# Kernel optimization log

Measured on AMD Instinct MI355X. Metric: run time of the kernel, lower is better.

## Reference

```python
import jax, jax.numpy as jnp
import numpy as np

B, L, U = 64, 512, 7          # batch, seq_len, enc_in
H = 128                        # hidden_dim
LAYERS = 2                     # num LSTM layers
PRED = 96                      # pred_len
EPS = 1e-5


def setup_inputs() -> dict:
    key = jax.random.key(0)
    ks = jax.random.split(key, 9)
    s = 0.05  # small param scale for numerical sanity
    return {
        "x": jax.random.normal(ks[0], (B, L, U), dtype=jnp.float32),
        "emb_W": jax.random.normal(ks[1], (H, 1), dtype=jnp.float32) * s,
        "emb_b": jax.random.normal(ks[2], (H,), dtype=jnp.float32) * s,
        "Wih": jax.random.normal(ks[3], (LAYERS, 4 * H, H), dtype=jnp.float32) * s,
        "Whh": jax.random.normal(ks[4], (LAYERS, 4 * H, H), dtype=jnp.float32) * s,
        "bih": jax.random.normal(ks[5], (LAYERS, 4 * H), dtype=jnp.float32) * s,
        "bhh": jax.random.normal(ks[6], (LAYERS, 4 * H), dtype=jnp.float32) * s,
        "fc_W": jax.random.normal(ks[7], (PRED, H), dtype=jnp.float32) * s,
        "fc_b": jax.random.normal(ks[8], (PRED,), dtype=jnp.float32) * s,
    }


def _lstm_layer(x, Wih, Whh, bih, bhh):
    """PyTorch-semantics single LSTM layer. x: [N, L, H_in] -> [N, L, H]."""
    N = x.shape[0]
    Hh = Whh.shape[1]
    # precompute input projections for all timesteps: [N, L, 4H]
    xp = jnp.einsum('nli,gi->nlg', x, Wih) + bih + bhh
    xp = jnp.swapaxes(xp, 0, 1)  # [L, N, 4H] for scan over time

    def step(carry, xt):
        h, c = carry
        gates = xt + h @ Whh.T           # [N, 4H]
        i, f, g, o = jnp.split(gates, 4, axis=-1)  # torch gate order i,f,g,o
        i = jax.nn.sigmoid(i)
        f = jax.nn.sigmoid(f)
        g = jnp.tanh(g)
        o = jax.nn.sigmoid(o)
        c = f * c + i * g
        h = o * jnp.tanh(c)
        return (h, c), h

    h0 = jnp.zeros((N, Hh), x.dtype)
    (_, _), hs = jax.lax.scan(step, (h0, h0), xp)
    return jnp.swapaxes(hs, 0, 1)  # [N, L, H]


def reference(x, emb_W, emb_b, Wih, Whh, bih, bhh, fc_W, fc_b):
    Bn, Ln, Un = x.shape
    # per-channel instance norm over time (stats detached in original)
    means = jax.lax.stop_gradient(jnp.mean(x, axis=1, keepdims=True))          # [B,1,U]
    stdev = jax.lax.stop_gradient(jnp.sqrt(jnp.var(x, axis=1, keepdims=True) + EPS))
    xn = (x - means) / stdev
    # NOTE: original does a raw row-major reshape (no channel permute); replicate exactly.
    xs = xn.reshape(Bn * Un, Ln, 1)                                            # [B*U, L, 1]
    h = xs @ emb_W.T + emb_b                                                   # [B*U, L, H]
    for l in range(Wih.shape[0]):
        h = _lstm_layer(h, Wih[l], Whh[l], bih[l], bhh[l])
    out = h[:, -1, :] @ fc_W.T + fc_b                                          # [B*U, PRED]
    out = out.reshape(Bn, -1, Un)                                              # [B, PRED, U]
    return out * stdev + means
```

## Files before the change

### kernel.cpp

```cpp
#include <hip/hip_runtime.h>
#include <stdint.h>

typedef short bf16x8 __attribute__((ext_vector_type(8)));
typedef float f32x4  __attribute__((ext_vector_type(4)));

#define HH 128
#define NN 448
#define PREDN 96

#define OFF_MEAN 0
#define OFF_STD  448
#define OFF_A    896
#define OFF_B0   1408
#define OFF_B1   1920
#define OFF_H1   2432
#define OFF_XSB  59776
#define OFF_WPK  174464

#define L2E  1.442695041f
#define L2E2 2.885390082f

#define ROWB 592
#define BUFB 9472

__device__ __forceinline__ float bflo(uint32_t w){ union{uint32_t u; float f;} v; v.u = w<<16; return v.f; }
__device__ __forceinline__ float bfhi(uint32_t w){ union{uint32_t u; float f;} v; v.u = w & 0xffff0000u; return v.f; }

static __device__ __forceinline__ uint32_t packbf2(float a, float b){
    union { float f; uint32_t u; } ua, ub; ua.f = a; ub.f = b;
    uint32_t x = ua.u, y = ub.u;
    uint32_t lo = (x + 0x7fffu + ((x>>16)&1u)) >> 16;
    uint32_t hi = (y + 0x7fffu + ((y>>16)&1u)) >> 16;
    return (lo & 0xffffu) | (hi<<16);
}
static __device__ __forceinline__ uint16_t bfr(float f){
    union { float f; uint32_t u; } v; v.f = f;
    return (uint16_t)((v.u + 0x7fffu + ((v.u>>16)&1u)) >> 16);
}

#if __has_builtin(__builtin_amdgcn_exp2f)
#define EXP2(x) __builtin_amdgcn_exp2f(x)
#else
#define EXP2(x) __expf(0.69314718056f*(x))
#endif
#if __has_builtin(__builtin_amdgcn_rcpf)
#define RCPF(x) __builtin_amdgcn_rcpf(x)
#else
#define RCPF(x) (1.0f/(x))
#endif

__device__ __forceinline__ float sig2(float x){ return RCPF(1.f + EXP2(-x)); }
__device__ __forceinline__ float tanh2(float xs){ return fmaf(-2.f, RCPF(EXP2(xs) + 1.f), 1.f); }

__global__ void stats_k(const float* __restrict__ x, float* __restrict__ ws){
    int bu = blockIdx.x;
    int b = bu / 7, u = bu % 7;
    int i = threadIdx.x;
    const float* p = x + b*3584 + u;
    float s = 0.f, q = 0.f;
    #pragma unroll
    for (int m=0;m<8;m++){ float v = p[(i + 64*m)*7]; s += v; q += v*v; }
    for (int o=32;o>0;o>>=1){ s += __shfl_down(s,o); q += __shfl_down(q,o); }
    if (i==0){
        float mean = s * (1.f/512.f);
        float var  = q * (1.f/512.f) - mean*mean;
        ws[OFF_MEAN + bu] = mean;
        ws[OFF_STD  + bu] = sqrtf(var + 1e-5f);
    }
}

__global__ void norm_k(const float* __restrict__ x, float* __restrict__ ws){
    int i = blockIdx.x*256 + threadIdx.x;
    int b = i / 3584, u = i % 7;
    float m = ws[OFF_MEAN + b*7 + u];
    float sd = ws[OFF_STD + b*7 + u];
    float v = (x[i] - m) / sd;
    int np = i >> 9, tp = i & 511;
    uint16_t* xb = (uint16_t*)(ws + OFF_XSB);
    xb[(np>>4)*8192 + tp*16 + (np&15)] = (uint16_t)(packbf2(v, 0.f) & 0xffffu);
}

__global__ void prep_k(const float* __restrict__ Wih, const float* __restrict__ embW,
                       const float* __restrict__ embb, const float* __restrict__ bih,
                       const float* __restrict__ bhh, float* __restrict__ ws){
    int g = threadIdx.x;
    const float* wr = Wih + g*HH;
    float a = 0.f, bb = 0.f;
    #pragma unroll 4
    for (int k=0;k<HH;k++){ a += wr[k]*embW[k]; bb += wr[k]*embb[k]; }
    ws[OFF_A  + g] = a;
    ws[OFF_B0 + g] = bb + bih[g] + bhh[g];
    ws[OFF_B1 + g] = bih[512 + g] + bhh[512 + g];
}

__global__ void prep2_k(const float* __restrict__ Whh, const float* __restrict__ Wih,
                        float* __restrict__ ws){
    int idx = blockIdx.x*256 + threadIdx.x;
    int lane = idx & 63;
    int sg = idx >> 6;
    int wvmt = sg / 13, slot = sg % 13;
    int gp  = wvmt*16 + (lane&15);
    int type = gp & 3, unit = gp >> 2;
    int row = type*128 + unit;
    float S = (type==2) ? L2E2 : L2E;
    uint4 r;
    if (slot == 4){
        r.x = r.y = r.z = r.w = 0u;
        if ((lane>>4) == 0) r.x = packbf2(ws[OFF_A+row]*S, ws[OFF_B0+row]*S);
    } else {
        const float* src; int kk;
        if (slot < 4)      { src = Whh + row*128;         kk = slot;   }
        else if (slot < 9) { src = Wih + 65536 + row*128; kk = slot-5; }
        else               { src = Whh + 65536 + row*128; kk = slot-9; }
        int k0 = kk*32 + (lane>>4)*8;
        r.x = packbf2(src[k0]*S,   src[k0+1]*S);
        r.y = packbf2(src[k0+2]*S, src[k0+3]*S);
        r.z = packbf2(src[k0+4]*S, src[k0+5]*S);
        r.w = packbf2(src[k0+6]*S, src[k0+7]*S);
    }
    ((uint4*)(ws + OFF_WPK))[sg*64 + lane] = r;
}

union FragU { bf16x8 v; uint4 q; };

__device__ __forceinline__ f32x4 mm(bf16x8 a, bf16x8 b, f32x4 c){
    return __builtin_amdgcn_mfma_f32_16x16x32_bf16(a, b, c, 0, 0, 0);
}
#define LD(p) (*(const bf16x8*)(p))

__global__ __launch_bounds__(512, 2) void lstm_core(float* __restrict__ ws)
{
    __shared__ uint16_t xsT[8192];
    __shared__ __align__(16) uint16_t hbuf[2*BUFB/2];

    const int tid = threadIdx.x;
    const int wv = tid>>6, l = tid&63;
    const int r   = l & 15;
    const int q16 = (l>>4)*16;
    const int bx = blockIdx.x, n0 = bx*16;
    char* hb = (char*)hbuf;

    const uint16_t* xb = (const uint16_t*)(ws + OFF_XSB) + bx*8192;
    for (int i=tid;i<8192;i+=512) xsT[i] = xb[i];
    for (int i=tid;i<BUFB;i+=512) hbuf[i] = 0;
    __syncthreads();
    if (tid < 32){
        int bsel = tid>>4, rr = tid&15;
        *(uint16_t*)(hb + bsel*BUFB + rr*ROWB + 514) = 0x3F80;
    }
    if (tid < 16){
        *(uint16_t*)(hb + tid*ROWB + 512) = xsT[tid];
    }

    bf16x8 wL0[4][5], wI1[4][4], wH1[4][4];
    uint32_t b1pk[4][2];
    const uint4* wpk = (const uint4*)(ws + OFF_WPK);
    #pragma unroll
    for (int mt=0;mt<4;++mt){
        int base = ((wv*4+mt)*13)*64 + l;
        #pragma unroll
        for (int kk=0;kk<5;kk++){ FragU u; u.q = wpk[base + kk*64];     wL0[mt][kk]=u.v; }
        #pragma unroll
        for (int kk=0;kk<4;kk++){ FragU u; u.q = wpk[base + (5+kk)*64]; wI1[mt][kk]=u.v; }
        #pragma unroll
        for (int kk=0;kk<4;kk++){ FragU u; u.q = wpk[base + (9+kk)*64]; wH1[mt][kk]=u.v; }
        int uu = (wv*4+mt)*4 + (l>>4);
        b1pk[mt][0] = packbf2(ws[OFF_B1+uu]*L2E,      ws[OFF_B1+128+uu]*L2E);
        b1pk[mt][1] = packbf2(ws[OFF_B1+256+uu]*L2E2, ws[OFF_B1+384+uu]*L2E);
    }

    float c0[4]={0,0,0,0}, c1[4]={0,0,0,0};
    const int rbase = r*ROWB + q16;
    const int wbase = r*ROWB + wv*32 + 2*(l>>4);

    __syncthreads();

    for (int t=0;t<512;++t){
        const int co = (t&1)*BUFB;
        const int no = BUFB - co;
        const char* pc = hb + co + rbase;
        const char* pn = hb + no + rbase;
        char* pw = hb + no + wbase;

        {
            bf16x8 f0 = LD(pc+0), f1 = LD(pc+64), f2 = LD(pc+128), f3 = LD(pc+192), fa = LD(pc+512);
            f32x4 a0={0,0,0,0}, a1={0,0,0,0}, a2={0,0,0,0}, a3={0,0,0,0};
            a0=mm(wL0[0][0],f0,a0); a1=mm(wL0[1][0],f0,a1); a2=mm(wL0[2][0],f0,a2); a3=mm(wL0[3][0],f0,a3);
            a0=mm(wL0[0][1],f1,a0); a1=mm(wL0[1][1],f1,a1); a2=mm(wL0[2][1],f1,a2); a3=mm(wL0[3][1],f1,a3);
            a0=mm(wL0[0][2],f2,a0); a1=mm(wL0[1][2],f2,a1); a2=mm(wL0[2][2],f2,a2); a3=mm(wL0[3][2],f2,a3);
            a0=mm(wL0[0][3],f3,a0); a1=mm(wL0[1][3],f3,a1); a2=mm(wL0[2][3],f3,a2); a3=mm(wL0[3][3],f3,a3);
            a0=mm(wL0[0][4],fa,a0); a1=mm(wL0[1][4],fa,a1); a2=mm(wL0[2][4],fa,a2); a3=mm(wL0[3][4],fa,a3);
            #pragma unroll
            for (int mt=0;mt<4;++mt){
                f32x4 a = (mt==0)?a0:(mt==1)?a1:(mt==2)?a2:a3;
                float i_ = sig2(a[0]);
                float f_ = sig2(a[1]);
                float g_ = tanh2(a[2]);
                float o_ = sig2(a[3]);
                float cn = fmaf(f_, c0[mt], i_*g_);
                c0[mt] = cn;
                float h = o_ * tanh2(cn*L2E2);
                *(uint16_t*)(pw + 8*mt) = bfr(h);
            }
        }
        __syncthreads();

        {
            bf16x8 g0 = LD(pn+0),   g1 = LD(pn+64),  g2 = LD(pn+128), g3 = LD(pn+192);
            bf16x8 v0 = LD(pc+256), v1 = LD(pc+320), v2 = LD(pc+384), v3 = LD(pc+448);
            f32x4 a0={0,0,0,0}, a1={0,0,0,0}, a2={0,0,0,0}, a3={0,0,0,0};
            a0=mm(wI1[0][0],g0,a0); a1=mm(wI1[1][0],g0,a1); a2=mm(wI1[2][0],g0,a2); a3=mm(wI1[3][0],g0,a3);
            a0=mm(wI1[0][1],g1,a0); a1=mm(wI1[1][1],g1,a1); a2=mm(wI1[2][1],g1,a2); a3=mm(wI1[3][1],g1,a3);
            a0=mm(wI1[0][2],g2,a0); a1=mm(wI1[1][2],g2,a1); a2=mm(wI1[2][2],g2,a2); a3=mm(wI1[3][2],g2,a3);
            a0=mm(wI1[0][3],g3,a0); a1=mm(wI1[1][3],g3,a1); a2=mm(wI1[2][3],g3,a2); a3=mm(wI1[3][3],g3,a3);
            a0=mm(wH1[0][0],v0,a0); a1=mm(wH1[1][0],v0,a1); a2=mm(wH1[2][0],v0,a2); a3=mm(wH1[3][0],v0,a3);
            a0=mm(wH1[0][1],v1,a0); a1=mm(wH1[1][1],v1,a1); a2=mm(wH1[2][1],v1,a2); a3=mm(wH1[3][1],v1,a3);
            a0=mm(wH1[0][2],v2,a0); a1=mm(wH1[1][2],v2,a1); a2=mm(wH1[2][2],v2,a2); a3=mm(wH1[3][2],v2,a3);
            a0=mm(wH1[0][3],v3,a0); a1=mm(wH1[1][3],v3,a1); a2=mm(wH1[2][3],v3,a2); a3=mm(wH1[3][3],v3,a3);
            #pragma unroll
            for (int mt=0;mt<4;++mt){
                f32x4 a = (mt==0)?a0:(mt==1)?a1:(mt==2)?a2:a3;
                float i_ = sig2(a[0] + bflo(b1pk[mt][0]));
                float f_ = sig2(a[1] + bfhi(b1pk[mt][0]));
                float g_ = tanh2(a[2] + bflo(b1pk[mt][1]));
                float o_ = sig2(a[3] + bfhi(b1pk[mt][1]));
                float cn = fmaf(f_, c1[mt], i_*g_);
                c1[mt] = cn;
                float h = o_ * tanh2(cn*L2E2);
                *(uint16_t*)(pw + 256 + 8*mt) = bfr(h);
                if (t==511) ws[OFF_H1 + (n0+r)*128 + (wv*16 + mt*4 + (l>>4))] = h;
            }
        }
        if (wv==0 && l<16){
            *(uint16_t*)(hb + no + l*ROWB + 512) = xsT[((t+1)&511)*16 + l];
        }
        __syncthreads();
    }
}

__global__ void out_k(const float* __restrict__ fcW, const float* __restrict__ fcb,
                      const float* __restrict__ ws, float* __restrict__ out){
    __shared__ float hl[128];
    int n = blockIdx.x, tid = threadIdx.x;
    hl[tid] = ws[OFF_H1 + n*128 + tid];
    __syncthreads();
    if (tid < PREDN){
        float acc = fcb[tid];
        const float* wr = fcW + tid*128;
        #pragma unroll 4
        for (int k=0;k<128;k++) acc += wr[k]*hl[k];
        int idx = n*PREDN + tid;
        int b = idx / 672, u = idx % 7;
        out[idx] = acc * ws[OFF_STD + b*7 + u] + ws[OFF_MEAN + b*7 + u];
    }
}

extern "C" void kernel_launch(void* const* d_in, const int* in_sizes, int n_in,
                              void* d_out, int out_size, void* d_ws, size_t ws_size,
                              hipStream_t stream)
{
    const float* x    = (const float*)d_in[0];
    const float* embW = (const float*)d_in[1];
    const float* embb = (const float*)d_in[2];
    const float* Wih  = (const float*)d_in[3];
    const float* Whh  = (const float*)d_in[4];
    const float* bih  = (const float*)d_in[5];
    const float* bhh  = (const float*)d_in[6];
    const float* fcW  = (const float*)d_in[7];
    const float* fcb  = (const float*)d_in[8];
    float* ws  = (float*)d_ws;
    float* out = (float*)d_out;

    stats_k<<<448, 64, 0, stream>>>(x, ws);
    norm_k<<<896, 256, 0, stream>>>(x, ws);
    prep_k<<<1, 512, 0, stream>>>(Wih, embW, embb, bih, bhh, ws);
    prep2_k<<<104, 256, 0, stream>>>(Whh, Wih, ws);
    lstm_core<<<28, 512, 0, stream>>>(ws);
    out_k<<<NN, 128, 0, stream>>>(fcW, fcb, ws, out);
}
```

Measured before the change: 1.003 ms.

## Skew LSTM layers by one timestep to remove per-step barrier

Layer 1 now processes timestep t-1 while layer 0 processes timestep t, so both read the same current h buffer and one __syncthreads per step is dropped. A separate epilogue finishes the last layer-1 step and writes the final hidden state. It also adds s_setprio around the MFMA blocks and a sched_barrier to steer instruction scheduling. The risk is correctness at the skew boundaries: the t==0 layer-1 update is skipped and the final step is handled outside the loop.

```diff
diff --git a/kernel.cpp b/kernel.cpp
--- a/kernel.cpp
+++ b/kernel.cpp
@@ -131,7 +131,7 @@
 __global__ __launch_bounds__(512, 2) void lstm_core(float* __restrict__ ws)
 {
     __shared__ uint16_t xsT[8192];
-    __shared__ __align__(16) uint16_t hbuf[2*BUFB/2];
+    __shared__ __align__(16) uint16_t hbuf[BUFB];
 
     const int tid = threadIdx.x;
     const int wv = tid>>6, l = tid&63;
@@ -179,47 +179,50 @@
         const int co = (t&1)*BUFB;
         const int no = BUFB - co;
         const char* pc = hb + co + rbase;
-        const char* pn = hb + no + rbase;
         char* pw = hb + no + wbase;
 
-        {
-            bf16x8 f0 = LD(pc+0), f1 = LD(pc+64), f2 = LD(pc+128), f3 = LD(pc+192), fa = LD(pc+512);
-            f32x4 a0={0,0,0,0}, a1={0,0,0,0}, a2={0,0,0,0}, a3={0,0,0,0};
-            a0=mm(wL0[0][0],f0,a0); a1=mm(wL0[1][0],f0,a1); a2=mm(wL0[2][0],f0,a2); a3=mm(wL0[3][0],f0,a3);
-            a0=mm(wL0[0][1],f1,a0); a1=mm(wL0[1][1],f1,a1); a2=mm(wL0[2][1],f1,a2); a3=mm(wL0[3][1],f1,a3);
-            a0=mm(wL0[0][2],f2,a0); a1=mm(wL0[1][2],f2,a1); a2=mm(wL0[2][2],f2,a2); a3=mm(wL0[3][2],f2,a3);
-            a0=mm(wL0[0][3],f3,a0); a1=mm(wL0[1][3],f3,a1); a2=mm(wL0[2][3],f3,a2); a3=mm(wL0[3][3],f3,a3);
-            a0=mm(wL0[0][4],fa,a0); a1=mm(wL0[1][4],fa,a1); a2=mm(wL0[2][4],fa,a2); a3=mm(wL0[3][4],fa,a3);
+        bf16x8 f0 = LD(pc+0), f1 = LD(pc+64), f2 = LD(pc+128), f3 = LD(pc+192);
+        f32x4 b0={0,0,0,0}, b1={0,0,0,0}, b2={0,0,0,0}, b3={0,0,0,0};
+        __builtin_amdgcn_s_setprio(1);
+        b0=mm(wI1[0][0],f0,b0); b1=mm(wI1[1][0],f0,b1); b2=mm(wI1[2][0],f0,b2); b3=mm(wI1[3][0],f0,b3);
+        b0=mm(wI1[0][1],f1,b0); b1=mm(wI1[1][1],f1,b1); b2=mm(wI1[2][1],f1,b2); b3=mm(wI1[3][1],f1,b3);
+        b0=mm(wI1[0][2],f2,b0); b1=mm(wI1[1][2],f2,b1); b2=mm(wI1[2][2],f2,b2); b3=mm(wI1[3][2],f2,b3);
+        b0=mm(wI1[0][3],f3,b0); b1=mm(wI1[1][3],f3,b1); b2=mm(wI1[2][3],f3,b2); b3=mm(wI1[3][3],f3,b3);
+        bf16x8 fa = LD(pc+512);
+        f32x4 a0={0,0,0,0}, a1={0,0,0,0}, a2={0,0,0,0}, a3={0,0,0,0};
+        a0=mm(wL0[0][0],f0,a0); a1=mm(wL0[1][0],f0,a1); a2=mm(wL0[2][0],f0,a2); a3=mm(wL0[3][0],f0,a3);
+        a0=mm(wL0[0][1],f1,a0); a1=mm(wL0[1][1],f1,a1); a2=mm(wL0[2][1],f1,a2); a3=mm(wL0[3][1],f1,a3);
+        a0=mm(wL0[0][2],f2,a0); a1=mm(wL0[1][2],f2,a1); a2=mm(wL0[2][2],f2,a2); a3=mm(wL0[3][2],f2,a3);
+        a0=mm(wL0[0][3],f3,a0); a1=mm(wL0[1][3],f3,a1); a2=mm(wL0[2][3],f3,a2); a3=mm(wL0[3][3],f3,a3);
+        a0=mm(wL0[0][4],fa,a0); a1=mm(wL0[1][4],fa,a1); a2=mm(wL0[2][4],fa,a2); a3=mm(wL0[3][4],fa,a3);
+        __builtin_amdgcn_s_setprio(0);
+
+        #pragma unroll
+        for (int mt=0;mt<4;++mt){
+            f32x4 a = (mt==0)?a0:(mt==1)?a1:(mt==2)?a2:a3;
+            float i_ = sig2(a[0]);
+            float f_ = sig2(a[1]);
+            float g_ = tanh2(a[2]);
+            float o_ = sig2(a[3]);
+            float cn = fmaf(f_, c0[mt], i_*g_);
+            c0[mt] = cn;
+            float h = o_ * tanh2(cn*L2E2);
+            *(uint16_t*)(pw + 8*mt) = bfr(h);
+        }
+
+        __builtin_amdgcn_sched_barrier(0);
+        bf16x8 v0 = LD(pc+256), v1 = LD(pc+320), v2 = LD(pc+384), v3 = LD(pc+448);
+        __builtin_amdgcn_s_setprio(1);
+        b0=mm(wH1[0][0],v0,b0); b1=mm(wH1[1][0],v0,b1); b2=mm(wH1[2][0],v0,b2); b3=mm(wH1[3][0],v0,b3);
+        b0=mm(wH1[0][1],v1,b0); b1=mm(wH1[1][1],v1,b1); b2=mm(wH1[2][1],v1,b2); b3=mm(wH1[3][1],v1,b3);
+        b0=mm(wH1[0][2],v2,b0); b1=mm(wH1[1][2],v2,b1); b2=mm(wH1[2][2],v2,b2); b3=mm(wH1[3][2],v2,b3);
+        b0=mm(wH1[0][3],v3,b0); b1=mm(wH1[1][3],v3,b1); b2=mm(wH1[2][3],v3,b2); b3=mm(wH1[3][3],v3,b3);
+        __builtin_amdgcn_s_setprio(0);
+
+        if (t){
             #pragma unroll
             for (int mt=0;mt<4;++mt){
-                f32x4 a = (mt==0)?a0:(mt==1)?a1:(mt==2)?a2:a3;
-                float i_ = sig2(a[0]);
-                float f_ = sig2(a[1]);
-                float g_ = tanh2(a[2]);
-                float o_ = sig2(a[3]);
-                float cn = fmaf(f_, c0[mt], i_*g_);
-                c0[mt] = cn;
-                float h = o_ * tanh2(cn*L2E2);
-                *(uint16_t*)(pw + 8*mt) = bfr(h);
-            }
-        }
-        __syncthreads();
-
-        {
-            bf16x8 g0 = LD(pn+0),   g1 = LD(pn+64),  g2 = LD(pn+128), g3 = LD(pn+192);
-            bf16x8 v0 = LD(pc+256), v1 = LD(pc+320), v2 = LD(pc+384), v3 = LD(pc+448);
-            f32x4 a0={0,0,0,0}, a1={0,0,0,0}, a2={0,0,0,0}, a3={0,0,0,0};
-            a0=mm(wI1[0][0],g0,a0); a1=mm(wI1[1][0],g0,a1); a2=mm(wI1[2][0],g0,a2); a3=mm(wI1[3][0],g0,a3);
-            a0=mm(wI1[0][1],g1,a0); a1=mm(wI1[1][1],g1,a1); a2=mm(wI1[2][1],g1,a2); a3=mm(wI1[3][1],g1,a3);
-            a0=mm(wI1[0][2],g2,a0); a1=mm(wI1[1][2],g2,a1); a2=mm(wI1[2][2],g2,a2); a3=mm(wI1[3][2],g2,a3);
-            a0=mm(wI1[0][3],g3,a0); a1=mm(wI1[1][3],g3,a1); a2=mm(wI1[2][3],g3,a2); a3=mm(wI1[3][3],g3,a3);
-            a0=mm(wH1[0][0],v0,a0); a1=mm(wH1[1][0],v0,a1); a2=mm(wH1[2][0],v0,a2); a3=mm(wH1[3][0],v0,a3);
-            a0=mm(wH1[0][1],v1,a0); a1=mm(wH1[1][1],v1,a1); a2=mm(wH1[2][1],v1,a2); a3=mm(wH1[3][1],v1,a3);
-            a0=mm(wH1[0][2],v2,a0); a1=mm(wH1[1][2],v2,a1); a2=mm(wH1[2][2],v2,a2); a3=mm(wH1[3][2],v2,a3);
-            a0=mm(wH1[0][3],v3,a0); a1=mm(wH1[1][3],v3,a1); a2=mm(wH1[2][3],v3,a2); a3=mm(wH1[3][3],v3,a3);
-            #pragma unroll
-            for (int mt=0;mt<4;++mt){
-                f32x4 a = (mt==0)?a0:(mt==1)?a1:(mt==2)?a2:a3;
+                f32x4 a = (mt==0)?b0:(mt==1)?b1:(mt==2)?b2:b3;
                 float i_ = sig2(a[0] + bflo(b1pk[mt][0]));
                 float f_ = sig2(a[1] + bfhi(b1pk[mt][0]));
                 float g_ = tanh2(a[2] + bflo(b1pk[mt][1]));
@@ -228,13 +231,38 @@
                 c1[mt] = cn;
                 float h = o_ * tanh2(cn*L2E2);
                 *(uint16_t*)(pw + 256 + 8*mt) = bfr(h);
-                if (t==511) ws[OFF_H1 + (n0+r)*128 + (wv*16 + mt*4 + (l>>4))] = h;
             }
         }
         if (wv==0 && l<16){
             *(uint16_t*)(hb + no + l*ROWB + 512) = xsT[((t+1)&511)*16 + l];
         }
         __syncthreads();
+    }
+
+    {
+        const char* pc = hb + rbase;
+        bf16x8 f0 = LD(pc+0),   f1 = LD(pc+64),  f2 = LD(pc+128), f3 = LD(pc+192);
+        bf16x8 v0 = LD(pc+256), v1 = LD(pc+320), v2 = LD(pc+384), v3 = LD(pc+448);
+        f32x4 b0={0,0,0,0}, b1={0,0,0,0}, b2={0,0,0,0}, b3={0,0,0,0};
+        b0=mm(wI1[0][0],f0,b0); b1=mm(wI1[1][0],f0,b1); b2=mm(wI1[2][0],f0,b2); b3=mm(wI1[3][0],f0,b3);
+        b0=mm(wI1[0][1],f1,b0); b1=mm(wI1[1][1],f1,b1); b2=mm(wI1[2][1],f1,b2); b3=mm(wI1[3][1],f1,b3);
+        b0=mm(wI1[0][2],f2,b0); b1=mm(wI1[1][2],f2,b1); b2=mm(wI1[2][2],f2,b2); b3=mm(wI1[3][2],f2,b3);
+        b0=mm(wI1[0][3],f3,b0); b1=mm(wI1[1][3],f3,b1); b2=mm(wI1[2][3],f3,b2); b3=mm(wI1[3][3],f3,b3);
+        b0=mm(wH1[0][0],v0,b0); b1=mm(wH1[1][0],v0,b1); b2=mm(wH1[2][0],v0,b2); b3=mm(wH1[3][0],v0,b3);
+        b0=mm(wH1[0][1],v1,b0); b1=mm(wH1[1][1],v1,b1); b2=mm(wH1[2][1],v1,b2); b3=mm(wH1[3][1],v1,b3);
+        b0=mm(wH1[0][2],v2,b0); b1=mm(wH1[1][2],v2,b1); b2=mm(wH1[2][2],v2,b2); b3=mm(wH1[3][2],v2,b3);
+        b0=mm(wH1[0][3],v3,b0); b1=mm(wH1[1][3],v3,b1); b2=mm(wH1[2][3],v3,b2); b3=mm(wH1[3][3],v3,b3);
+        #pragma unroll
+        for (int mt=0;mt<4;++mt){
+            f32x4 a = (mt==0)?b0:(mt==1)?b1:(mt==2)?b2:b3;
+            float i_ = sig2(a[0] + bflo(b1pk[mt][0]));
+            float f_ = sig2(a[1] + bfhi(b1pk[mt][0]));
+            float g_ = tanh2(a[2] + bflo(b1pk[mt][1]));
+            float o_ = sig2(a[3] + bfhi(b1pk[mt][1]));
+            float cn = fmaf(f_, c1[mt], i_*g_);
+            float h = o_ * tanh2(cn*L2E2);
+            ws[OFF_H1 + (n0+r)*128 + (wv*16 + mt*4 + (l>>4))] = h;
+        }
     }
 }
 
```

Result: slower. 1.132 ms (+12.9%).
